# Kernel optimization log

Measured on AMD Instinct MI355X. Metric: run time of the kernel, lower is better.

## Reference

```python
import jax, jax.numpy as jnp
import numpy as np

L = 4          # n_layers
A = 4          # aspect heads: causal, intentional, temporal, normative
D = 1024       # d_model
DK = D // A    # 256
S = 3072
NE, NA = 1536, 1024  # n_events, n_agents (norms = S - NE - NA)
EPS = 1e-5


def _layernorm(x, g, b):
    mu = jnp.mean(x, axis=-1, keepdims=True)
    var = jnp.mean(jnp.square(x - mu), axis=-1, keepdims=True)
    return g * (x - mu) * jax.lax.rsqrt(var + EPS) + b


def setup_inputs() -> dict:
    key = jax.random.key(0)
    ks = jax.random.split(key, 12)
    s = 0.02
    return {
        "hidden": jax.random.normal(ks[0], (1, S, D), jnp.float32),
        "Wq": jax.random.normal(ks[1], (L, D, D), jnp.float32) * s,
        "bq": jnp.zeros((L, D), jnp.float32),
        "Wk": jax.random.normal(ks[2], (L, D, D), jnp.float32) * s,
        "bk": jnp.zeros((L, D), jnp.float32),
        "Wv": jax.random.normal(ks[3], (L, D, D), jnp.float32) * s,
        "bv": jnp.zeros((L, D), jnp.float32),
        "Wh": jax.random.normal(ks[4], (L, A, D, DK), jnp.float32) * s,
        "bh": jnp.zeros((L, A, DK), jnp.float32),
        "Wo": jax.random.normal(ks[5], (L, D, D), jnp.float32) * s,
        "bo": jnp.zeros((L, D), jnp.float32),
        "g1": jnp.ones((L, D), jnp.float32),
        "b1n": jnp.zeros((L, D), jnp.float32),
        "g2": jnp.ones((L, D), jnp.float32),
        "b2n": jnp.zeros((L, D), jnp.float32),
        "Wf1": jax.random.normal(ks[6], (L, D, 2 * D), jnp.float32) * s,
        "bf1": jnp.zeros((L, 2 * D), jnp.float32),
        "Wf2": jax.random.normal(ks[7], (L, 2 * D, D), jnp.float32) * s,
        "bf2": jnp.zeros((L, D), jnp.float32),
        "Whead": jax.random.normal(ks[8], (4, D), jnp.float32) * s,  # guilt, causation, intention, harm
        "bhead": jnp.zeros((4,), jnp.float32),
        "n_events": NE,
        "n_agents": NA,
    }


def reference(hidden, Wq, bq, Wk, bk, Wv, bv, Wh, bh, Wo, bo,
              g1, b1n, g2, b2n, Wf1, bf1, Wf2, bf2, Whead, bhead,
              n_events, n_agents):
    scale = 1.0 / np.sqrt(DK).astype(np.float32)
    h = hidden  # [B, S, D]
    for l in range(L):
        Q = h @ Wq[l] + bq[l]
        K = h @ Wk[l] + bk[l]
        V = h @ Wv[l] + bv[l]
        # per-aspect projections: [B, A, S, DK]
        Qh = jnp.einsum('bsd,ade->base', Q, Wh[l]) + bh[l][None, :, None, :]
        Kh = jnp.einsum('bsd,ade->base', K, Wh[l]) + bh[l][None, :, None, :]
        Vh = jnp.einsum('bsd,ade->base', V, Wh[l]) + bh[l][None, :, None, :]
        scores = jnp.einsum('base,bate->bast', Qh, Kh) * scale  # [B, A, S, S]
        attn = jax.nn.softmax(scores, axis=-1)  # dropout = identity (eval)
        ctx = jnp.einsum('bast,bate->base', attn, Vh)  # [B, A, S, DK]
        B = ctx.shape[0]
        ctx = ctx.transpose(0, 2, 1, 3).reshape(B, S, D)  # concat aspect heads
        attn_out = ctx @ Wo[l] + bo[l]
        h = _layernorm(h + attn_out, g1[l], b1n[l])
        ffn = jax.nn.relu(h @ Wf1[l] + bf1[l]) @ Wf2[l] + bf2[l]
        h = _layernorm(h + ffn, g2[l], b2n[l])
    event_h = h[:, :n_events, :]
    agent_h = h[:, n_events:n_events + n_agents, :]
    guilt = agent_h @ Whead[0] + bhead[0]      # [B, n_agents]
    causation = agent_h @ Whead[1] + bhead[1]
    intention = agent_h @ Whead[2] + bhead[2]
    harm = event_h @ Whead[3] + bhead[3]       # [B, n_events]
    return jnp.concatenate([guilt, causation, intention, harm], axis=-1)
```

## Files before the change

kernel.cpp:

```cpp
#include <hip/hip_runtime.h>
#include <cstdint>

typedef unsigned short u16;
typedef __bf16  bf16x8 __attribute__((ext_vector_type(8)));
typedef float   f32x4  __attribute__((ext_vector_type(4)));
typedef unsigned short u16x4 __attribute__((ext_vector_type(4)));
typedef unsigned short u16x8 __attribute__((ext_vector_type(8)));

#define S_LEN 3072
#define DMODEL 1024

__device__ __forceinline__ float bf2f(u16 u){ return __uint_as_float(((unsigned)u) << 16); }
__device__ __forceinline__ u16 f2bf(float f){
    unsigned u = __float_as_uint(f);
    return (u16)((u + 0x7fffu + ((u >> 16) & 1u)) >> 16);
}
__device__ __forceinline__ u16 cvld(const void* p, long i, int mode){
    return mode ? f2bf(((const float*)p)[i]) : ((const u16*)p)[i];
}

__device__ __forceinline__ void async16(const void* g, void* l){
    __builtin_amdgcn_global_load_lds(
        (const __attribute__((address_space(1))) unsigned int*)g,
        (__attribute__((address_space(3))) unsigned int*)l, 16, 0, 0);
}

__global__ void sniff_kernel(const u16* __restrict__ x, int* __restrict__ flag)
{
    __shared__ int r[256];
    int tid = threadIdx.x, w = 0;
    for (int j = tid; j < 4096; j += 256){
        int e = (x[j] >> 7) & 0xFF;
        if (e < 90 || e > 140) w++;
    }
    r[tid] = w; __syncthreads();
    for (int s = 128; s > 0; s >>= 1){ if (tid < s) r[tid] += r[tid + s]; __syncthreads(); }
    if (tid == 0){ flag[0] = (r[0] > 256) ? 1 : 0; flag[1] = 0; }
}


__global__ __launch_bounds__(256)
void gemm_scores(const u16* __restrict__ A, int lda,
                 const u16* __restrict__ B, int ldb,
                 u16* __restrict__ C, int ldc,
                 float* __restrict__ rowSums,
                 int K, long aBS, long bBS, long cBS)
{
    __shared__ __align__(16) u16 smem[2 * 128 * 64];
    u16* Abuf = smem;
    u16* Bbuf = smem + 128 * 64;
    const int tid  = threadIdx.x;
    const int lane = tid & 63, wid = tid >> 6;
    const int wm = wid >> 1, wn = wid & 1;
    const int quad = lane >> 4, lr = lane & 15;
    const int jx = lr & 7;
    const int bat = blockIdx.z;

    A += (long)bat * aBS + (long)blockIdx.x * 128 * lda;
    B += (long)bat * bBS + (long)blockIdx.y * 128 * ldb;

    f32x4 zero = {0.f, 0.f, 0.f, 0.f};
    f32x4 acc[4][4];
#pragma unroll
    for (int i = 0; i < 4; i++)
#pragma unroll
        for (int j = 0; j < 4; j++) acc[i][j] = zero;

    const u16* aP[4]; const u16* bP[4]; int ldst[4];
#pragma unroll
    for (int i = 0; i < 4; i++){
        int u = i * 256 + tid;
        int m = u >> 3, c = u & 7;
        int cs = c ^ (m & 7);
        aP[i] = A + (long)m * lda + cs * 8;
        bP[i] = B + (long)m * ldb + cs * 8;
        ldst[i] = u * 8;
    }

    const int kTiles = K >> 6;
    for (int kt = 0; kt < kTiles; ++kt){
        const int k0 = kt << 6;
        __syncthreads();
#pragma unroll
        for (int i = 0; i < 4; i++) async16(aP[i] + k0, Abuf + ldst[i]);
#pragma unroll
        for (int i = 0; i < 4; i++) async16(bP[i] + k0, Bbuf + ldst[i]);
        __syncthreads();
#pragma unroll
        for (int ks = 0; ks < 2; ++ks){
            const int j = (ks * 4 + quad) ^ jx;
            bf16x8 af[4], bfg[4];
#pragma unroll
            for (int t = 0; t < 4; t++){
                int m  = wm * 64 + t * 16 + lr;
                af[t]  = *(const bf16x8*)(Abuf + (m * 8 + j) * 8);
                int n  = wn * 64 + t * 16 + lr;
                bfg[t] = *(const bf16x8*)(Bbuf + (n * 8 + j) * 8);
            }
#pragma unroll
            for (int mt = 0; mt < 4; mt++)
#pragma unroll
                for (int nt = 0; nt < 4; nt++)
                    acc[mt][nt] = __builtin_amdgcn_mfma_f32_16x16x32_bf16(
                        af[mt], bfg[nt], acc[mt][nt], 0, 0, 0);
        }
    }

    const int rowBase = blockIdx.x * 128 + wm * 64;
    const int colBase = blockIdx.y * 128 + wn * 64;
    const float scale = 0.0625f;
    float* scw = (float*)smem + (size_t)wid * (16 * 68);
    const int row_l = lane >> 2, cq = lane & 3;

    __syncthreads();
#pragma unroll
    for (int mt = 0; mt < 4; ++mt){
#pragma unroll
        for (int nt = 0; nt < 4; nt++)
#pragma unroll
            for (int r = 0; r < 4; r++)
                scw[(quad * 4 + r) * 68 + nt * 16 + lr] = acc[mt][nt][r];
        float vals[16];
#pragma unroll
        for (int j = 0; j < 4; j++)
            *(f32x4*)(vals + j * 4) = *(const f32x4*)(scw + row_l * 68 + cq * 16 + j * 4);
        float rs = 0.f;
        u16x8 pk0, pk1;
#pragma unroll
        for (int i = 0; i < 16; i++){
            float e = __expf(vals[i] * scale);
            rs += e;
            if (i < 8) pk0[i] = f2bf(e); else pk1[i - 8] = f2bf(e);
        }
        rs += __shfl_xor(rs, 1, 64);
        rs += __shfl_xor(rs, 2, 64);
        int row_g = rowBase + mt * 16 + row_l;
        if (cq == 0) atomicAdd(&rowSums[(long)bat * S_LEN + row_g], rs);
        u16* cp = C + (long)bat * cBS + (long)row_g * ldc + colBase + cq * 16;
        *(u16x8*)cp       = pk0;
        *(u16x8*)(cp + 8) = pk1;
    }
}

template<int SPLIT, int MODE>
__global__ __launch_bounds__(256)
void gemm128(const u16* __restrict__ A, int lda,
             const u16* __restrict__ B, int ldb,
             void* __restrict__ Cv, int ldc,
             const u16* __restrict__ bias,
             int K, long aBS, long bBS, long cBS, long pStride,
             const float* __restrict__ rs)
{
    __shared__ __align__(16) u16 smem[4 * 128 * 64];
    u16* As0 = smem;
    u16* Bs0 = smem + 2 * 128 * 64;
    const int tid  = threadIdx.x;
    const int lane = tid & 63, wid = tid >> 6;
    const int wm = wid >> 1, wn = wid & 1;
    const int quad = lane >> 4, lr = lane & 15;
    const int jx = lr & 7;

    const int z   = blockIdx.z;
    const int bat = z / SPLIT;
    const int sp  = z % SPLIT;
    const int kLen = K / SPLIT;

    A += (long)bat * aBS + (long)blockIdx.x * 128 * lda + (long)sp * kLen;
    B += (long)bat * bBS + (long)blockIdx.y * 128 * ldb + (long)sp * kLen;

    f32x4 zero = {0.f, 0.f, 0.f, 0.f};
    f32x4 acc[4][4];
#pragma unroll
    for (int i = 0; i < 4; i++)
#pragma unroll
        for (int j = 0; j < 4; j++) acc[i][j] = zero;

    const u16* aP[4]; const u16* bP[4]; int ldst[4];
#pragma unroll
    for (int i = 0; i < 4; i++){
        int u = i * 256 + tid;
        int m = u >> 3, c = u & 7;
        int cs = c ^ (m & 7);
        aP[i] = A + (long)m * lda + cs * 8;
        bP[i] = B + (long)m * ldb + cs * 8;
        ldst[i] = u * 8;
    }

    auto stage = [&](int kt, int b){
        const int k0 = kt << 6;
        u16* Ad = As0 + b * (128 * 64);
        u16* Bd = Bs0 + b * (128 * 64);
#pragma unroll
        for (int i = 0; i < 4; i++) async16(aP[i] + k0, Ad + ldst[i]);
#pragma unroll
        for (int i = 0; i < 4; i++) async16(bP[i] + k0, Bd + ldst[i]);
    };

    const int kTiles = kLen >> 6;
    stage(0, 0);
    __syncthreads();
    for (int kt = 0; kt < kTiles; ++kt){
        const int cur = kt & 1;
        if (kt + 1 < kTiles) stage(kt + 1, cur ^ 1);
        const u16* Ac = As0 + cur * (128 * 64);
        const u16* Bc = Bs0 + cur * (128 * 64);
#pragma unroll
        for (int ks = 0; ks < 2; ++ks){
            const int j = (ks * 4 + quad) ^ jx;
            bf16x8 af[4], bfg[4];
#pragma unroll
            for (int t = 0; t < 4; t++){
                int m  = wm * 64 + t * 16 + lr;
                af[t]  = *(const bf16x8*)(Ac + (m * 8 + j) * 8);
                int n  = wn * 64 + t * 16 + lr;
                bfg[t] = *(const bf16x8*)(Bc + (n * 8 + j) * 8);
            }
#pragma unroll
            for (int mt = 0; mt < 4; mt++)
#pragma unroll
                for (int nt = 0; nt < 4; nt++)
                    acc[mt][nt] = __builtin_amdgcn_mfma_f32_16x16x32_bf16(
                        af[mt], bfg[nt], acc[mt][nt], 0, 0, 0);
        }
        __syncthreads();
    }

    const int rowBase = blockIdx.x * 128 + wm * 64;
    const int colBase = blockIdx.y * 128 + wn * 64;
    const int slabw = colBase >> 10;

    if (MODE == 1 && slabw == 2){
        u16* scw = smem + (size_t)wid * (16 * 72);
        const int e_l = lane >> 2, sh = lane & 3;
#pragma unroll
        for (int nt = 0; nt < 4; nt++){
            float bv2 = bf2f(bias[colBase + nt * 16 + lr]);
#pragma unroll
            for (int mt = 0; mt < 4; mt++){
                u16x4 pk;
#pragma unroll
                for (int r = 0; r < 4; r++) pk[r] = f2bf(acc[mt][nt][r] + bv2);
                *(u16x4*)(scw + lr * 72 + mt * 16 + quad * 4) = pk;
            }
            const int e_g = (colBase & 1023) + nt * 16 + e_l;
            u16* dst = (u16*)Cv + (long)2 * S_LEN * DMODEL + (long)e_g * S_LEN
                     + rowBase + sh * 16;
            *(u16x8*)(dst)     = *(const u16x8*)(scw + e_l * 72 + sh * 16);
            *(u16x8*)(dst + 8) = *(const u16x8*)(scw + e_l * 72 + sh * 16 + 8);
        }
        return;
    }

    float* scw = (float*)smem + (size_t)wid * (16 * 68);
    const int row_l = lane >> 2, cq = lane & 3;
#pragma unroll
    for (int mt = 0; mt < 4; ++mt){
#pragma unroll
        for (int nt = 0; nt < 4; nt++)
#pragma unroll
            for (int r = 0; r < 4; r++)
                scw[(quad * 4 + r) * 68 + nt * 16 + lr] = acc[mt][nt][r];
        float vals[16];
#pragma unroll
        for (int j = 0; j < 4; j++)
            *(f32x4*)(vals + j * 4) = *(const f32x4*)(scw + row_l * 68 + cq * 16 + j * 4);
        const int row_g = rowBase + mt * 16 + row_l;
        const int colg  = colBase + cq * 16;
        float inv = 1.f;
        if (MODE == 3) inv = 1.f / rs[(long)bat * S_LEN + row_g];
        float bv[16];
        if (SPLIT == 1 && MODE != 3 && bias){
            u16x8 b0 = *(const u16x8*)(bias + colg);
            u16x8 b1 = *(const u16x8*)(bias + colg + 8);
#pragma unroll
            for (int i = 0; i < 8; i++){ bv[i] = bf2f(b0[i]); bv[8 + i] = bf2f(b1[i]); }
        } else {
#pragma unroll
            for (int i = 0; i < 16; i++) bv[i] = 0.f;
        }
        u16x8 pk0, pk1;
#pragma unroll
        for (int i = 0; i < 16; i++){
            float v = vals[i] + bv[i];
            if (MODE == 2) v = fmaxf(v, 0.f);
            if (MODE == 3) v *= inv;
            if (i < 8) pk0[i] = f2bf(v); else pk1[i - 8] = f2bf(v);
        }
        long idx;
        if (SPLIT > 1)      idx = (long)sp * pStride + (long)bat * cBS + (long)row_g * ldc + colg;
        else if (MODE == 1) idx = ((long)slabw * S_LEN + row_g) * DMODEL + (colg & 1023);
        else                idx = (long)bat * cBS + (long)row_g * ldc + colg;
        u16* cp = (u16*)Cv + idx;
        *(u16x8*)cp       = pk0;
        *(u16x8*)(cp + 8) = pk1;
    }
}

__global__ __launch_bounds__(256)
void wprep(const int* __restrict__ flag, int l,
           const void* Wo, const void* Wf1, const void* Wf2, const void* Wh,
           const void* Wq, const void* Wk, const void* Wv,
           u16* __restrict__ WoT, u16* __restrict__ Wf1T,
           u16* __restrict__ Wf2T, u16* __restrict__ WhT,
           u16* __restrict__ Wcat, float* __restrict__ rowSums)
{
    const int mode = *flag;
    const int z = blockIdx.x;
    const int tx = threadIdx.x, ty = threadIdx.y;

    if (z >= 7680){
        int idx = (z - 7680) * 256 + ty * 32 + tx;
        rowSums[idx] = 0.f;
        return;
    }
    if (z >= 6144){
        int t = ty * 32 + tx;
        long base = (long)(z - 6144) * 2048;
#pragma unroll
        for (int j = 0; j < 8; j++){
            long g = base + j * 256 + t;
            int slab = (int)(g >> 20);
            long r = g & 1048575;
            const void* src = (slab == 0) ? Wq : (slab == 1) ? Wk : Wv;
            Wcat[g] = cvld(src, (long)l * 1048576 + r, mode);
        }
        return;
    }

    const void* in; u16* out; long ib; int R, C, rb, cb;
    if (z < 1024){
        in = Wo; out = WoT; ib = (long)l * 1048576; R = 1024; C = 1024;
        cb = z & 31; rb = z >> 5;
    } else if (z < 3072){
        int t = z - 1024;
        in = Wf1; out = Wf1T; ib = (long)l * 2097152; R = 1024; C = 2048;
        cb = t & 63; rb = t >> 6;
    } else if (z < 5120){
        int t = z - 3072;
        in = Wf2; out = Wf2T; ib = (long)l * 2097152; R = 2048; C = 1024;
        cb = t & 31; rb = t >> 5;
    } else {
        int t = z - 5120;
        int a = t >> 8, u = t & 255;
        in = Wh; out = WhT + (long)a * 262144;
        ib = (long)l * 1048576 + (long)a * 262144; R = 1024; C = 256;
        cb = u & 7; rb = u >> 3;
    }

    __shared__ u16 tbuf[32][34];
    int r0 = rb * 32, c0 = cb * 32;
#pragma unroll
    for (int j = 0; j < 4; j++){
        int r = r0 + ty + j * 8;
        tbuf[ty + j * 8][tx] = cvld(in, ib + (long)r * C + c0 + tx, mode);
    }
    __syncthreads();
#pragma unroll
    for (int j = 0; j < 4; j++){
        int c = c0 + ty + j * 8;
        out[(long)c * R + r0 + tx] = tbuf[tx][ty + j * 8];
    }
}

__global__ __launch_bounds__(256)
void init_h(const int* __restrict__ flag, const void* __restrict__ hin,
            float* __restrict__ h, u16* __restrict__ hbf)
{
    const int mode = *flag;
    long i = (long)blockIdx.x * 256 + threadIdx.x;
    u16 u = cvld(hin, i, mode);
    h[i]   = bf2f(u);
    hbf[i] = u;
}

#define OFF_BQKV 0
#define OFF_BH   12288
#define OFF_BO   16384
#define OFF_BF1  20480
#define OFF_BF2  28672
#define OFF_G1   32768
#define OFF_B1N  36864
#define OFF_G2   40960
#define OFF_B2N  45056
#define OFF_WHD  49152
#define OFF_BHD  53248
#define BIAS_TOT 53252

__global__ __launch_bounds__(256)
void cvt_biases(const int* __restrict__ flag,
                const void* bq, const void* bk, const void* bv, const void* bh,
                const void* bo, const void* bf1, const void* bf2,
                const void* g1, const void* b1n, const void* g2, const void* b2n,
                const void* whd, const void* bhd, u16* __restrict__ A)
{
    int i = blockIdx.x * 256 + threadIdx.x;
    if (i >= BIAS_TOT) return;
    const int mode = *flag;
    u16 v;
    if (i < OFF_BH){
        int l = i / 3072, r = i % 3072;
        const void* p = (r < 1024) ? bq : (r < 2048) ? bk : bv;
        v = cvld(p, (long)l * 1024 + (r & 1023), mode);
    }
    else if (i < OFF_BO)  v = cvld(bh,  i - OFF_BH, mode);
    else if (i < OFF_BF1) v = cvld(bo,  i - OFF_BO, mode);
    else if (i < OFF_BF2) v = cvld(bf1, i - OFF_BF1, mode);
    else if (i < OFF_G1)  v = cvld(bf2, i - OFF_BF2, mode);
    else if (i < OFF_B1N) v = cvld(g1,  i - OFF_G1, mode);
    else if (i < OFF_G2)  v = cvld(b1n, i - OFF_B1N, mode);
    else if (i < OFF_B2N) v = cvld(g2,  i - OFF_G2, mode);
    else if (i < OFF_WHD) v = cvld(b2n, i - OFF_B2N, mode);
    else if (i < OFF_BHD) v = cvld(whd, i - OFF_WHD, mode);
    else                  v = cvld(bhd, i - OFF_BHD, mode);
    A[i] = v;
}

__global__ __launch_bounds__(256)
void bias_combine(const u16* __restrict__ arena, const u16* __restrict__ WhT,
                  int l, u16* __restrict__ bqkvh)
{
    int i = blockIdx.x * 256 + threadIdx.x;
    int z = i >> 10, n = i & 1023;
    const u16* bz = arena + OFF_BQKV + l * 3072 + z * 1024;
    const u16* wr = WhT + (long)n * 1024;
    float s = bf2f(arena[OFF_BH + l * 1024 + n]);
    for (int d = 0; d < 1024; d += 8){
        bf16x8 w = *(const bf16x8*)(wr + d);
        bf16x8 b = *(const bf16x8*)(bz + d);
#pragma unroll
        for (int j = 0; j < 8; j++) s += (float)w[j] * (float)b[j];
    }
    bqkvh[i] = f2bf(s);
}

__device__ __forceinline__ float blockSum(float v, float* red){
    int lane = threadIdx.x & 63, wid = threadIdx.x >> 6;
#pragma unroll
    for (int o = 32; o > 0; o >>= 1) v += __shfl_down(v, o, 64);
    __syncthreads();
    if (lane == 0) red[wid] = v;
    __syncthreads();
    return red[0] + red[1] + red[2] + red[3];
}

__global__ __launch_bounds__(256)
void ln_fused(float* __restrict__ h, const u16* __restrict__ parts, long pStride,
              int nparts, const u16* __restrict__ bias, u16* __restrict__ hbf,
              const u16* __restrict__ g, const u16* __restrict__ b)
{
    __shared__ float red[4];
    long base = (long)blockIdx.x * DMODEL;
    int tid = threadIdx.x;
    float v[4];
    float s = 0.f;
#pragma unroll
    for (int j = 0; j < 4; j++){
        int c = tid + j * 256;
        float x = bf2f(bias[c]);
        for (int sp = 0; sp < nparts; sp++) x += bf2f(parts[(long)sp * pStride + base + c]);
        float r = h[base + c] + x;
        v[j] = r; s += r;
    }
    float mu = blockSum(s, red) * (1.f / DMODEL);
    float s2 = 0.f;
#pragma unroll
    for (int j = 0; j < 4; j++){ float d = v[j] - mu; s2 += d * d; }
    float var = blockSum(s2, red) * (1.f / DMODEL);
    float inv = rsqrtf(var + 1e-5f);
#pragma unroll
    for (int j = 0; j < 4; j++){
        int c = tid + j * 256;
        float y = (v[j] - mu) * inv * bf2f(g[c]) + bf2f(b[c]);
        h[base + c]   = y;
        hbf[base + c] = f2bf(y);
    }
}

__global__ __launch_bounds__(256)
void head_kernel(const int* __restrict__ flag, const float* __restrict__ h,
                 const u16* __restrict__ arena, const int* __restrict__ nePtr,
                 const int* __restrict__ naPtr, void* __restrict__ outp)
{
    __shared__ float red[4];
    int o = blockIdx.x;
    int ne = *nePtr, na = *naPtr;
    int widx, row;
    if (o < 3 * na){ widx = o / na; row = ne + o % na; }
    else           { widx = 3;      row = o - 3 * na; }
    int tid = threadIdx.x;
    const float* hr = h + (long)row * DMODEL;
    const u16*   w  = arena + OFF_WHD + widx * DMODEL;
    float s = 0.f;
#pragma unroll
    for (int j = 0; j < 4; j++){ int c = tid + j * 256; s += hr[c] * bf2f(w[c]); }
    s = blockSum(s, red);
    if (tid == 0){
        float r = s + bf2f(arena[OFF_BHD + widx]);
        if (*flag) ((float*)outp)[o] = r;
        else       ((u16*)outp)[o]   = f2bf(r);
    }
}

extern "C" void kernel_launch(void* const* d_in, const int* in_sizes, int n_in,
                              void* d_out, int out_size, void* d_ws, size_t ws_size,
                              hipStream_t stream)
{
    const void* hidden = d_in[0];
    const void* Wq  = d_in[1];  const void* bq  = d_in[2];
    const void* Wk  = d_in[3];  const void* bk  = d_in[4];
    const void* Wv  = d_in[5];  const void* bv  = d_in[6];
    const void* Wh  = d_in[7];  const void* bh  = d_in[8];
    const void* Wo  = d_in[9];  const void* bo  = d_in[10];
    const void* g1  = d_in[11]; const void* b1n = d_in[12];
    const void* g2  = d_in[13]; const void* b2n = d_in[14];
    const void* Wf1 = d_in[15]; const void* bf1 = d_in[16];
    const void* Wf2 = d_in[17]; const void* bf2 = d_in[18];
    const void* Whd = d_in[19]; const void* bhd = d_in[20];
    const int* nePtr = (const int*)d_in[21];
    const int* naPtr = (const int*)d_in[22];

    const long D = 1024, S = 3072, L = 4, DK = 256;

    char* ws = (char*)d_ws;
    size_t off = 0;
    auto alloc = [&](size_t bytes)->char*{
        char* p = ws + off;
        off = (off + bytes + 255) & ~(size_t)255;
        return p;
    };
    int*  flag   = (int*)alloc(256);
    u16*  barena = (u16*)alloc(BIAS_TOT * 2);
    u16*  bqkvh  = (u16*)alloc(3 * D * 2);
    float* rowSums = (float*)alloc(4 * S * 4);
    u16*  WhT    = (u16*)alloc(D * D * 2);
    u16*  WqkvhT = (u16*)alloc(3 * D * D * 2);
    u16*  WoT    = (u16*)alloc(D * D * 2);
    u16*  Wf1T   = (u16*)alloc(2 * D * D * 2);
    u16*  Wf2T   = (u16*)alloc(2 * D * D * 2);
    float* h     = (float*)alloc(S * D * 4);
    u16*  hbf    = (u16*)alloc(S * D * 2);
    u16*  qkvh   = (u16*)alloc(3 * S * D * 2);
    u16*  ctx    = (u16*)alloc(S * D * 2);
    size_t baseEnd = off;

    size_t reg4 = (size_t)4 * S * S * 2;
    size_t reg1 = (size_t)S * S * 2 + (size_t)S * 2 * D * 2;
    int HBv = (ws_size >= baseEnd + reg4 + 4096) ? 4 : 1;
    char* regionB = alloc(HBv == 4 ? reg4 : reg1);

    u16* scoresP = (u16*)regionB;
    u16* Wcat    = (u16*)regionB;
    u16* woParts = (u16*)regionB;
    u16* ffn1;
    u16* f2Parts;
    if (HBv == 4){
        ffn1    = (u16*)regionB;
        f2Parts = (u16*)(regionB + (size_t)S * 2 * D * 2);
    } else {
        ffn1    = (u16*)(regionB + (size_t)S * S * 2);
        f2Parts = (u16*)regionB;
    }

    const long pSD = S * D;

    dim3 tb(32, 8);
    sniff_kernel<<<1, 256, 0, stream>>>((const u16*)hidden, flag);
    cvt_biases<<<(BIAS_TOT + 255) / 256, 256, 0, stream>>>(
        flag, bq, bk, bv, bh, bo, bf1, bf2, g1, b1n, g2, b2n, Whd, bhd, barena);
    init_h<<<(int)(S * D / 256), 256, 0, stream>>>(flag, hidden, h, hbf);

    for (int l = 0; l < L; ++l){
        wprep<<<7728, tb, 0, stream>>>(flag, l, Wo, Wf1, Wf2, Wh, Wq, Wk, Wv,
                                       WoT, Wf1T, Wf2T, WhT, Wcat, rowSums);
        gemm128<1, 0><<<dim3(8, 8, 3), 256, 0, stream>>>(
            WhT, 1024, Wcat, 1024, WqkvhT, 1024, nullptr,
            1024, 0, (long)D * D, (long)D * D, 0, nullptr);
        bias_combine<<<12, 256, 0, stream>>>(barena, WhT, l, bqkvh);

        gemm128<1, 1><<<dim3(24, 24, 1), 256, 0, stream>>>(
            hbf, 1024, WqkvhT, 1024, qkvh, 0, bqkvh,
            1024, 0, 0, 0, 0, nullptr);

        if (HBv == 4){
            gemm_scores<<<dim3(24, 24, 4), 256, 0, stream>>>(
                qkvh, 1024, qkvh + S * D, 1024, scoresP, (int)S,
                rowSums, (int)DK, DK, DK, (long)S * S);
            gemm128<1, 3><<<dim3(24, 2, 4), 256, 0, stream>>>(
                scoresP, (int)S, qkvh + 2 * S * D, (int)S,
                ctx, 1024, nullptr, (int)S,
                (long)S * S, (long)DK * S, DK, 0, rowSums);
        } else {
            for (int h0 = 0; h0 < 4; ++h0){
                gemm_scores<<<dim3(24, 24, 1), 256, 0, stream>>>(
                    qkvh + h0 * DK, 1024, qkvh + S * D + h0 * DK, 1024,
                    scoresP, (int)S, rowSums + h0 * S, (int)DK, 0, 0, 0);
                gemm128<1, 3><<<dim3(24, 2, 1), 256, 0, stream>>>(
                    scoresP, (int)S, qkvh + 2 * S * D + (long)h0 * DK * S, (int)S,
                    ctx + h0 * DK, 1024, nullptr, (int)S,
                    0, 0, 0, 0, rowSums + h0 * S);
            }
        }

        gemm128<2, 0><<<dim3(24, 8, 2), 256, 0, stream>>>(
            ctx, 1024, WoT, 1024, woParts, 1024, nullptr,
            1024, 0, 0, 0, pSD, nullptr);
        ln_fused<<<3072, 256, 0, stream>>>(h, woParts, pSD, 2, barena + OFF_BO + l * D,
                                           hbf, barena + OFF_G1 + l * D, barena + OFF_B1N + l * D);
        gemm128<1, 2><<<dim3(24, 16, 1), 256, 0, stream>>>(
            hbf, 1024, Wf1T, 1024, ffn1, 2048, barena + OFF_BF1 + l * 2 * D,
            1024, 0, 0, 0, 0, nullptr);
        gemm128<2, 0><<<dim3(24, 8, 2), 256, 0, stream>>>(
            ffn1, 2048, Wf2T, 2048, f2Parts, 1024, nullptr,
            2048, 0, 0, 0, pSD, nullptr);
        ln_fused<<<3072, 256, 0, stream>>>(h, f2Parts, pSD, 2, barena + OFF_BF2 + l * D,
                                           hbf, barena + OFF_G2 + l * D, barena + OFF_B2N + l * D);
    }
    head_kernel<<<out_size, 256, 0, stream>>>(flag, h, barena, nePtr, naPtr, d_out);
}
```

Baseline: 1.193 ms.

## Double-buffer the scores GEMM LDS tiles and restructure the exp/rowsum epilogue

The attention-scores GEMM now issues the async global-to-LDS loads for the next K tile before computing on the current one, using two LDS buffers and one barrier per iteration instead of two. This overlaps memory latency with MFMA work at the cost of doubling LDS use, which may lower occupancy. The epilogue also changes: it applies exp in registers directly on the accumulators, reduces row sums with lane shuffles, and stages bf16 values rather than fp32 through LDS for the transposed stores. That halves LDS traffic in the epilogue.

New measurement: 1.179 ms. About the same (-1.1%).

```diff
diff --git a/kernel.cpp b/kernel.cpp
--- a/kernel.cpp
+++ b/kernel.cpp
@@ -46,9 +46,9 @@
                  float* __restrict__ rowSums,
                  int K, long aBS, long bBS, long cBS)
 {
-    __shared__ __align__(16) u16 smem[2 * 128 * 64];
-    u16* Abuf = smem;
-    u16* Bbuf = smem + 128 * 64;
+    __shared__ __align__(16) u16 smem[4 * 128 * 64];
+    u16* As0 = smem;
+    u16* Bs0 = smem + 2 * 128 * 64;
     const int tid  = threadIdx.x;
     const int lane = tid & 63, wid = tid >> 6;
     const int wm = wid >> 1, wn = wid & 1;
@@ -77,15 +77,24 @@
         ldst[i] = u * 8;
     }
 
+    auto stage = [&](int kt, int b){
+        const int k0 = kt << 6;
+        u16* Ad = As0 + b * (128 * 64);
+        u16* Bd = Bs0 + b * (128 * 64);
+#pragma unroll
+        for (int i = 0; i < 4; i++) async16(aP[i] + k0, Ad + ldst[i]);
+#pragma unroll
+        for (int i = 0; i < 4; i++) async16(bP[i] + k0, Bd + ldst[i]);
+    };
+
     const int kTiles = K >> 6;
+    stage(0, 0);
+    __syncthreads();
     for (int kt = 0; kt < kTiles; ++kt){
-        const int k0 = kt << 6;
-        __syncthreads();
-#pragma unroll
-        for (int i = 0; i < 4; i++) async16(aP[i] + k0, Abuf + ldst[i]);
-#pragma unroll
-        for (int i = 0; i < 4; i++) async16(bP[i] + k0, Bbuf + ldst[i]);
-        __syncthreads();
+        const int cur = kt & 1;
+        if (kt + 1 < kTiles) stage(kt + 1, cur ^ 1);
+        const u16* Ac = As0 + cur * (128 * 64);
+        const u16* Bc = Bs0 + cur * (128 * 64);
 #pragma unroll
         for (int ks = 0; ks < 2; ++ks){
             const int j = (ks * 4 + quad) ^ jx;
@@ -93,9 +102,9 @@
 #pragma unroll
             for (int t = 0; t < 4; t++){
                 int m  = wm * 64 + t * 16 + lr;
-                af[t]  = *(const bf16x8*)(Abuf + (m * 8 + j) * 8);
+                af[t]  = *(const bf16x8*)(Ac + (m * 8 + j) * 8);
                 int n  = wn * 64 + t * 16 + lr;
-                bfg[t] = *(const bf16x8*)(Bbuf + (n * 8 + j) * 8);
+                bfg[t] = *(const bf16x8*)(Bc + (n * 8 + j) * 8);
             }
 #pragma unroll
             for (int mt = 0; mt < 4; mt++)
@@ -104,41 +113,45 @@
                     acc[mt][nt] = __builtin_amdgcn_mfma_f32_16x16x32_bf16(
                         af[mt], bfg[nt], acc[mt][nt], 0, 0, 0);
         }
+        __syncthreads();
     }
 
     const int rowBase = blockIdx.x * 128 + wm * 64;
     const int colBase = blockIdx.y * 128 + wn * 64;
     const float scale = 0.0625f;
-    float* scw = (float*)smem + (size_t)wid * (16 * 68);
+    u16* scw = smem + (size_t)wid * (16 * 72);
     const int row_l = lane >> 2, cq = lane & 3;
 
-    __syncthreads();
 #pragma unroll
     for (int mt = 0; mt < 4; ++mt){
+        float ev[4][4];
 #pragma unroll
         for (int nt = 0; nt < 4; nt++)
 #pragma unroll
             for (int r = 0; r < 4; r++)
-                scw[(quad * 4 + r) * 68 + nt * 16 + lr] = acc[mt][nt][r];
-        float vals[16];
-#pragma unroll
-        for (int j = 0; j < 4; j++)
-            *(f32x4*)(vals + j * 4) = *(const f32x4*)(scw + row_l * 68 + cq * 16 + j * 4);
-        float rs = 0.f;
-        u16x8 pk0, pk1;
-#pragma unroll
-        for (int i = 0; i < 16; i++){
-            float e = __expf(vals[i] * scale);
-            rs += e;
-            if (i < 8) pk0[i] = f2bf(e); else pk1[i - 8] = f2bf(e);
-        }
-        rs += __shfl_xor(rs, 1, 64);
-        rs += __shfl_xor(rs, 2, 64);
+                ev[nt][r] = __expf(acc[mt][nt][r] * scale);
+#pragma unroll
+        for (int r = 0; r < 4; r++){
+            float rs = ev[0][r] + ev[1][r] + ev[2][r] + ev[3][r];
+            rs += __shfl_xor(rs, 1, 64);
+            rs += __shfl_xor(rs, 2, 64);
+            rs += __shfl_xor(rs, 4, 64);
+            rs += __shfl_xor(rs, 8, 64);
+            if (lr == 0)
+                atomicAdd(&rowSums[(long)bat * S_LEN + rowBase + mt * 16 + quad * 4 + r], rs);
+        }
+#pragma unroll
+        for (int nt = 0; nt < 4; nt++)
+#pragma unroll
+            for (int r = 0; r < 4; r++)
+                scw[(quad * 4 + r) * 72 + nt * 16 + lr] = f2bf(ev[nt][r]);
+        u16x8 pk0 = *(const u16x8*)(scw + row_l * 72 + cq * 16);
+        u16x8 pk1 = *(const u16x8*)(scw + row_l * 72 + cq * 16 + 8);
         int row_g = rowBase + mt * 16 + row_l;
-        if (cq == 0) atomicAdd(&rowSums[(long)bat * S_LEN + row_g], rs);
         u16* cp = C + (long)bat * cBS + (long)row_g * ldc + colBase + cq * 16;
         *(u16x8*)cp       = pk0;
         *(u16x8*)(cp + 8) = pk1;
+        __syncthreads();
     }
 }
 
```

## Fuse attention scores, softmax and PV into a single flash-style kernel

Applied to the files above, without the earlier changes.

Replaces the separate scores GEMM (which wrote exp'd scores to a 4×S×S bf16 buffer with atomic row sums) and the PV GEMM with one fused kernel per 32-query block and head. It streams K/V tiles through double-buffered LDS, computes exp scores, and accumulates P·V in registers, normalising by in-block row sums at the end. This removes the large HBM round-trip of the score matrix and the atomics. In exchange each block handles only 32 queries over 4 waves with about 135KB LDS, so there is little occupancy and K/V reuse across queries is lower. There is also no max-subtraction, matching the previous unstable exp.

After: 1.385 ms. +16.1%, slower.

```diff
diff --git a/kernel.cpp b/kernel.cpp
--- a/kernel.cpp
+++ b/kernel.cpp
@@ -40,105 +40,136 @@
 
 
 __global__ __launch_bounds__(256)
-void gemm_scores(const u16* __restrict__ A, int lda,
-                 const u16* __restrict__ B, int ldb,
-                 u16* __restrict__ C, int ldc,
-                 float* __restrict__ rowSums,
-                 int K, long aBS, long bBS, long cBS)
-{
-    __shared__ __align__(16) u16 smem[2 * 128 * 64];
-    u16* Abuf = smem;
-    u16* Bbuf = smem + 128 * 64;
+void fused_attn(const u16* __restrict__ qkvh, u16* __restrict__ ctx)
+{
+    __shared__ __align__(16) u16 smem[67840];
+    u16*  Pb  = smem + 65536;
+    float* rsb = (float*)(smem + 67584);
+
     const int tid  = threadIdx.x;
     const int lane = tid & 63, wid = tid >> 6;
-    const int wm = wid >> 1, wn = wid & 1;
     const int quad = lane >> 4, lr = lane & 15;
     const int jx = lr & 7;
-    const int bat = blockIdx.z;
-
-    A += (long)bat * aBS + (long)blockIdx.x * 128 * lda;
-    B += (long)bat * bBS + (long)blockIdx.y * 128 * ldb;
+    const int h = blockIdx.y;
+    const int qbase = blockIdx.x * 32;
+
+    const u16* Q  = qkvh + (long)qbase * DMODEL + h * 256;
+    const u16* K  = qkvh + (long)S_LEN * DMODEL + h * 256;
+    const u16* Vt = qkvh + (long)2 * S_LEN * DMODEL + (long)h * 256 * S_LEN;
+
+    bf16x8 qf[2][8];
+#pragma unroll
+    for (int mt = 0; mt < 2; ++mt)
+#pragma unroll
+        for (int ks = 0; ks < 8; ++ks)
+            qf[mt][ks] = *(const bf16x8*)(Q + (long)(mt*16 + lr) * DMODEL + (ks*4 + quad) * 8);
 
     f32x4 zero = {0.f, 0.f, 0.f, 0.f};
-    f32x4 acc[4][4];
-#pragma unroll
-    for (int i = 0; i < 4; i++)
-#pragma unroll
-        for (int j = 0; j < 4; j++) acc[i][j] = zero;
-
-    const u16* aP[4]; const u16* bP[4]; int ldst[4];
-#pragma unroll
-    for (int i = 0; i < 4; i++){
+    f32x4 oa[2][4];
+#pragma unroll
+    for (int mt = 0; mt < 2; ++mt)
+#pragma unroll
+        for (int nt = 0; nt < 4; ++nt) oa[mt][nt] = zero;
+    float rsp[2][4] = {{0.f,0.f,0.f,0.f},{0.f,0.f,0.f,0.f}};
+
+    const u16* kP[8]; const u16* vP[8]; int dOf[8];
+#pragma unroll
+    for (int i = 0; i < 8; ++i){
         int u = i * 256 + tid;
-        int m = u >> 3, c = u & 7;
-        int cs = c ^ (m & 7);
-        aP[i] = A + (long)m * lda + cs * 8;
-        bP[i] = B + (long)m * ldb + cs * 8;
-        ldst[i] = u * 8;
-    }
-
-    const int kTiles = K >> 6;
-    for (int kt = 0; kt < kTiles; ++kt){
-        const int k0 = kt << 6;
+        int kr = u >> 5, kc = u & 31;
+        kP[i] = K + (long)kr * DMODEL + (kc ^ (kr & 7)) * 8;
+        int vr = u >> 3, vc = u & 7;
+        vP[i] = Vt + (long)vr * S_LEN + (vc ^ (vr & 7)) * 8;
+        dOf[i] = u * 8;
+    }
+
+    auto stageKV = [&](int it, int b){
+        const int kv0 = it << 6;
+        u16* Kd = smem + b * 16384;
+        u16* Vd = smem + 32768 + b * 16384;
+#pragma unroll
+        for (int i = 0; i < 8; ++i) async16(kP[i] + (long)kv0 * DMODEL, Kd + dOf[i]);
+#pragma unroll
+        for (int i = 0; i < 8; ++i) async16(vP[i] + kv0, Vd + dOf[i]);
+    };
+
+    const float scale = 0.0625f;
+    stageKV(0, 0);
+    __syncthreads();
+    for (int it = 0; it < 48; ++it){
+        const int cur = it & 1;
+        if (it + 1 < 48) stageKV(it + 1, cur ^ 1);
+        const u16* Kc = smem + cur * 16384;
+        f32x4 sa0 = zero, sa1 = zero;
+#pragma unroll
+        for (int ks = 0; ks < 8; ++ks){
+            const int j = (ks*4 + quad) ^ jx;
+            bf16x8 kb = *(const bf16x8*)(Kc + (wid*16 + lr) * 256 + j*8);
+            sa0 = __builtin_amdgcn_mfma_f32_16x16x32_bf16(qf[0][ks], kb, sa0, 0, 0, 0);
+            sa1 = __builtin_amdgcn_mfma_f32_16x16x32_bf16(qf[1][ks], kb, sa1, 0, 0, 0);
+        }
+#pragma unroll
+        for (int mt = 0; mt < 2; ++mt){
+#pragma unroll
+            for (int r = 0; r < 4; ++r){
+                float e = __expf((mt ? sa1[r] : sa0[r]) * scale);
+                rsp[mt][r] += e;
+                int m = mt*16 + quad*4 + r;
+                Pb[m*64 + (((wid*2 + (lr >> 3)) ^ (m & 7)) * 8) + (lr & 7)] = f2bf(e);
+            }
+        }
         __syncthreads();
-#pragma unroll
-        for (int i = 0; i < 4; i++) async16(aP[i] + k0, Abuf + ldst[i]);
-#pragma unroll
-        for (int i = 0; i < 4; i++) async16(bP[i] + k0, Bbuf + ldst[i]);
+        const u16* Vc = smem + 32768 + cur * 16384;
+#pragma unroll
+        for (int ks = 0; ks < 2; ++ks){
+            const int j = (ks*4 + quad) ^ jx;
+            bf16x8 pa0 = *(const bf16x8*)(Pb + lr*64        + j*8);
+            bf16x8 pa1 = *(const bf16x8*)(Pb + (16 + lr)*64 + j*8);
+#pragma unroll
+            for (int nt = 0; nt < 4; ++nt){
+                bf16x8 vb = *(const bf16x8*)(Vc + (wid*64 + nt*16 + lr) * 64 + j*8);
+                oa[0][nt] = __builtin_amdgcn_mfma_f32_16x16x32_bf16(pa0, vb, oa[0][nt], 0, 0, 0);
+                oa[1][nt] = __builtin_amdgcn_mfma_f32_16x16x32_bf16(pa1, vb, oa[1][nt], 0, 0, 0);
+            }
+        }
         __syncthreads();
-#pragma unroll
-        for (int ks = 0; ks < 2; ++ks){
-            const int j = (ks * 4 + quad) ^ jx;
-            bf16x8 af[4], bfg[4];
-#pragma unroll
-            for (int t = 0; t < 4; t++){
-                int m  = wm * 64 + t * 16 + lr;
-                af[t]  = *(const bf16x8*)(Abuf + (m * 8 + j) * 8);
-                int n  = wn * 64 + t * 16 + lr;
-                bfg[t] = *(const bf16x8*)(Bbuf + (n * 8 + j) * 8);
-            }
-#pragma unroll
-            for (int mt = 0; mt < 4; mt++)
-#pragma unroll
-                for (int nt = 0; nt < 4; nt++)
-                    acc[mt][nt] = __builtin_amdgcn_mfma_f32_16x16x32_bf16(
-                        af[mt], bfg[nt], acc[mt][nt], 0, 0, 0);
-        }
-    }
-
-    const int rowBase = blockIdx.x * 128 + wm * 64;
-    const int colBase = blockIdx.y * 128 + wn * 64;
-    const float scale = 0.0625f;
-    float* scw = (float*)smem + (size_t)wid * (16 * 68);
+    }
+
+#pragma unroll
+    for (int mt = 0; mt < 2; ++mt)
+#pragma unroll
+        for (int r = 0; r < 4; ++r){
+            float v = rsp[mt][r];
+            v += __shfl_xor(v, 1, 64);
+            v += __shfl_xor(v, 2, 64);
+            v += __shfl_xor(v, 4, 64);
+            v += __shfl_xor(v, 8, 64);
+            if (lr == 0) rsb[wid*32 + mt*16 + quad*4 + r] = v;
+        }
+    __syncthreads();
+    float inv[2][4];
+#pragma unroll
+    for (int mt = 0; mt < 2; ++mt)
+#pragma unroll
+        for (int r = 0; r < 4; ++r){
+            int m = mt*16 + quad*4 + r;
+            inv[mt][r] = 1.f / (rsb[m] + rsb[32 + m] + rsb[64 + m] + rsb[96 + m]);
+        }
+
+    u16* scw = smem + (size_t)wid * (16 * 72);
     const int row_l = lane >> 2, cq = lane & 3;
-
-    __syncthreads();
-#pragma unroll
-    for (int mt = 0; mt < 4; ++mt){
-#pragma unroll
-        for (int nt = 0; nt < 4; nt++)
-#pragma unroll
-            for (int r = 0; r < 4; r++)
-                scw[(quad * 4 + r) * 68 + nt * 16 + lr] = acc[mt][nt][r];
-        float vals[16];
-#pragma unroll
-        for (int j = 0; j < 4; j++)
-            *(f32x4*)(vals + j * 4) = *(const f32x4*)(scw + row_l * 68 + cq * 16 + j * 4);
-        float rs = 0.f;
-        u16x8 pk0, pk1;
-#pragma unroll
-        for (int i = 0; i < 16; i++){
-            float e = __expf(vals[i] * scale);
-            rs += e;
-            if (i < 8) pk0[i] = f2bf(e); else pk1[i - 8] = f2bf(e);
-        }
-        rs += __shfl_xor(rs, 1, 64);
-        rs += __shfl_xor(rs, 2, 64);
-        int row_g = rowBase + mt * 16 + row_l;
-        if (cq == 0) atomicAdd(&rowSums[(long)bat * S_LEN + row_g], rs);
-        u16* cp = C + (long)bat * cBS + (long)row_g * ldc + colBase + cq * 16;
-        *(u16x8*)cp       = pk0;
-        *(u16x8*)(cp + 8) = pk1;
+#pragma unroll
+    for (int mt = 0; mt < 2; ++mt){
+#pragma unroll
+        for (int nt = 0; nt < 4; ++nt)
+#pragma unroll
+            for (int r = 0; r < 4; ++r)
+                scw[(quad*4 + r) * 72 + nt*16 + lr] = f2bf(oa[mt][nt][r] * inv[mt][r]);
+        u16x8 p0 = *(const u16x8*)(scw + row_l * 72 + cq * 16);
+        u16x8 p1 = *(const u16x8*)(scw + row_l * 72 + cq * 16 + 8);
+        u16* cp = ctx + (long)(qbase + mt*16 + row_l) * DMODEL + h * 256 + wid * 64 + cq * 16;
+        *(u16x8*)cp       = p0;
+        *(u16x8*)(cp + 8) = p1;
     }
 }
 
@@ -266,10 +297,8 @@
             *(f32x4*)(vals + j * 4) = *(const f32x4*)(scw + row_l * 68 + cq * 16 + j * 4);
         const int row_g = rowBase + mt * 16 + row_l;
         const int colg  = colBase + cq * 16;
-        float inv = 1.f;
-        if (MODE == 3) inv = 1.f / rs[(long)bat * S_LEN + row_g];
         float bv[16];
-        if (SPLIT == 1 && MODE != 3 && bias){
+        if (SPLIT == 1 && bias){
             u16x8 b0 = *(const u16x8*)(bias + colg);
             u16x8 b1 = *(const u16x8*)(bias + colg + 8);
 #pragma unroll
@@ -283,7 +312,6 @@
         for (int i = 0; i < 16; i++){
             float v = vals[i] + bv[i];
             if (MODE == 2) v = fmaxf(v, 0.f);
-            if (MODE == 3) v *= inv;
             if (i < 8) pk0[i] = f2bf(v); else pk1[i - 8] = f2bf(v);
         }
         long idx;
@@ -519,7 +547,7 @@
     const int* nePtr = (const int*)d_in[21];
     const int* naPtr = (const int*)d_in[22];
 
-    const long D = 1024, S = 3072, L = 4, DK = 256;
+    const long D = 1024, S = 3072, L = 4;
 
     char* ws = (char*)d_ws;
     size_t off = 0;
@@ -541,25 +569,12 @@
     u16*  hbf    = (u16*)alloc(S * D * 2);
     u16*  qkvh   = (u16*)alloc(3 * S * D * 2);
     u16*  ctx    = (u16*)alloc(S * D * 2);
-    size_t baseEnd = off;
-
-    size_t reg4 = (size_t)4 * S * S * 2;
-    size_t reg1 = (size_t)S * S * 2 + (size_t)S * 2 * D * 2;
-    int HBv = (ws_size >= baseEnd + reg4 + 4096) ? 4 : 1;
-    char* regionB = alloc(HBv == 4 ? reg4 : reg1);
-
-    u16* scoresP = (u16*)regionB;
+
+    char* regionB = alloc((size_t)S * 2 * D * 2 + 2 * (size_t)S * D * 2);
     u16* Wcat    = (u16*)regionB;
     u16* woParts = (u16*)regionB;
-    u16* ffn1;
-    u16* f2Parts;
-    if (HBv == 4){
-        ffn1    = (u16*)regionB;
-        f2Parts = (u16*)(regionB + (size_t)S * 2 * D * 2);
-    } else {
-        ffn1    = (u16*)(regionB + (size_t)S * S * 2);
-        f2Parts = (u16*)regionB;
-    }
+    u16* ffn1    = (u16*)regionB;
+    u16* f2Parts = (u16*)(regionB + (size_t)S * 2 * D * 2);
 
     const long pSD = S * D;
 
@@ -581,25 +596,7 @@
             hbf, 1024, WqkvhT, 1024, qkvh, 0, bqkvh,
             1024, 0, 0, 0, 0, nullptr);
 
-        if (HBv == 4){
-            gemm_scores<<<dim3(24, 24, 4), 256, 0, stream>>>(
-                qkvh, 1024, qkvh + S * D, 1024, scoresP, (int)S,
-                rowSums, (int)DK, DK, DK, (long)S * S);
-            gemm128<1, 3><<<dim3(24, 2, 4), 256, 0, stream>>>(
-                scoresP, (int)S, qkvh + 2 * S * D, (int)S,
-                ctx, 1024, nullptr, (int)S,
-                (long)S * S, (long)DK * S, DK, 0, rowSums);
-        } else {
-            for (int h0 = 0; h0 < 4; ++h0){
-                gemm_scores<<<dim3(24, 24, 1), 256, 0, stream>>>(
-                    qkvh + h0 * DK, 1024, qkvh + S * D + h0 * DK, 1024,
-                    scoresP, (int)S, rowSums + h0 * S, (int)DK, 0, 0, 0);
-                gemm128<1, 3><<<dim3(24, 2, 1), 256, 0, stream>>>(
-                    scoresP, (int)S, qkvh + 2 * S * D + (long)h0 * DK * S, (int)S,
-                    ctx + h0 * DK, 1024, nullptr, (int)S,
-                    0, 0, 0, 0, rowSums + h0 * S);
-            }
-        }
+        fused_attn<<<dim3(96, 4), 256, 0, stream>>>(qkvh, ctx);
 
         gemm128<2, 0><<<dim3(24, 8, 2), 256, 0, stream>>>(
             ctx, 1024, WoT, 1024, woParts, 1024, nullptr,
```
